# Performance work log

Hardware: AMD Instinct MI355X
Metric: run time of the kernel (lower is better)

The kernel has to match this reference:

```python
import jax, jax.numpy as jnp
import numpy as np
import math

B = 8; SEQ = 1000; C_IN = 32; D = 512; H = 8; DK = 64; DV = 64
DFF = 2048; NL = 4; ARY = 4; INNER = 5


def get_mask_np(seq_size, ary, inner):
    # full k-ary tree sizes (padded) and effective sizes per scale
    full = 1
    while full < seq_size:
        full *= ary
    all_size = [full]; effe = [seq_size]
    while all_size[-1] > 1:
        all_size.append(all_size[-1] // ary)
        effe.append(math.ceil(effe[-1] / ary))
    n = sum(all_size)
    allow = np.zeros((n, n), dtype=bool)
    w = inner // 2
    starts = np.concatenate([[0], np.cumsum(all_size)]).astype(int)
    # intra-scale local window
    for l, sz in enumerate(all_size):
        s = starts[l]
        for i in range(sz):
            lo = max(i - w, 0); hi = min(i + w + 1, sz)
            allow[s + i, s + lo:s + hi] = True
    # inter-scale parent<->children links
    for l in range(1, len(all_size)):
        s = starts[l]; ps = starts[l - 1]
        for i in range(all_size[l]):
            lo = ps + i * ary; hi = ps + (i + 1) * ary
            allow[s + i, lo:hi] = True
            allow[lo:hi, s + i] = True
    return allow, all_size, effe

ALLOW_NP, ALL_SIZE, EFFE_SIZE = get_mask_np(SEQ, ARY, INNER)
NTOT = sum(ALL_SIZE)   # 1365
DEPTH = len(ALL_SIZE)  # 6
OFFS = np.concatenate([[0], np.cumsum(ALL_SIZE)]).astype(int)


def sinusoid_pe(length, d):
    pos = np.arange(length)[:, None].astype(np.float64)
    i = np.arange(d)[None, :]
    ang = pos / np.power(10000.0, (2 * (i // 2)) / d)
    pe = np.zeros((length, d), np.float32)
    pe[:, 0::2] = np.sin(ang[:, 0::2]); pe[:, 1::2] = np.cos(ang[:, 1::2])
    return pe

PE_NP = sinusoid_pe(SEQ, D)


def layer_norm(x, s, b, eps=1e-5):
    m = x.mean(-1, keepdims=True)
    v = ((x - m) ** 2).mean(-1, keepdims=True)
    return (x - m) * jax.lax.rsqrt(v + eps) * s + b


def setup_inputs() -> dict:
    key = jax.random.key(0)
    ks = jax.random.split(key, 10)
    p = lambda k, shape, sc=0.02: jax.random.normal(k, shape, jnp.float32) * sc
    return {
        "x": jax.random.normal(ks[0], (B, SEQ, C_IN), jnp.float32),
        "conv_w": p(ks[1], (D, C_IN, 3), 0.05),
        "norm_s": jnp.ones((D,), jnp.float32), "norm_b": jnp.zeros((D,), jnp.float32),
        "wq": p(ks[2], (NL, D, H * DK)), "wk": p(ks[3], (NL, D, H * DK)),
        "wv": p(ks[4], (NL, D, H * DV)), "wo": p(ks[5], (NL, H * DV, D)),
        "ln1_s": jnp.ones((NL, D), jnp.float32), "ln1_b": jnp.zeros((NL, D), jnp.float32),
        "w1": p(ks[6], (NL, D, DFF)), "b1": jnp.zeros((NL, DFF), jnp.float32),
        "w2": p(ks[7], (NL, DFF, D)), "b2": jnp.zeros((NL, D), jnp.float32),
        "ln2_s": jnp.ones((NL, D), jnp.float32), "ln2_b": jnp.zeros((NL, D), jnp.float32),
    }


def reference(x, conv_w, norm_s, norm_b, wq, wk, wv, wo, ln1_s, ln1_b,
              w1, b1, w2, b2, ln2_s, ln2_b):
    allow = jnp.asarray(ALLOW_NP)        # [N,N] True = attend
    pe = jnp.asarray(PE_NP)              # [S,D]
    # --- DataEmbedding: conv1d(k=3, circular pad, no bias) + sinusoid PE ---
    xt = jnp.concatenate([x[:, -1:], x, x[:, :1]], axis=1)       # (B,S+2,C)
    emb = jax.lax.conv_general_dilated(
        xt, conv_w, (1,), 'VALID', dimension_numbers=('NWC', 'OIW', 'NWC'))
    emb = emb + pe[None]                                          # (B,S,D)
    # pad sequence to full-tree leaf count
    emb = jnp.pad(emb, ((0, 0), (0, ALL_SIZE[0] - SEQ), (0, 0)))  # (B,L0,D)
    # --- MaxPooling_Construct: pool by ary per level, concat, LayerNorm ---
    parts = [emb]
    cur = emb
    for lvl in range(DEPTH - 1):
        L = cur.shape[1]
        cur = cur.reshape(B, L // ARY, ARY, D).max(axis=2)
        parts.append(cur)
    seq = jnp.concatenate(parts, axis=1)                          # (B,N,D)
    seq = layer_norm(seq, norm_s, norm_b)
    # --- masked MHA encoder layers (post-norm) ---
    scale = 1.0 / math.sqrt(DK)
    neg = jnp.float32(-1e9)
    for l in range(NL):
        q = (seq @ wq[l]).reshape(B, NTOT, H, DK)
        k = (seq @ wk[l]).reshape(B, NTOT, H, DK)
        v = (seq @ wv[l]).reshape(B, NTOT, H, DV)
        scores = jnp.einsum('bnhd,bmhd->bhnm', q, k) * scale
        scores = jnp.where(allow[None, None], scores, neg)
        attn = jax.nn.softmax(scores, axis=-1)
        ctx = jnp.einsum('bhnm,bmhd->bnhd', attn, v).reshape(B, NTOT, H * DV)
        seq = layer_norm(seq + ctx @ wo[l], ln1_s[l], ln1_b[l])
        ff = jax.nn.gelu(seq @ w1[l] + b1[l], approximate=False) @ w2[l] + b2[l]
        seq = layer_norm(seq + ff, ln2_s[l], ln2_b[l])
    # --- keep only the effective (unpadded) prefix of each scale ---
    out = jnp.concatenate(
        [seq[:, OFFS[i]:OFFS[i] + EFFE_SIZE[i]] for i in range(DEPTH)], axis=1)
    return out  # (B, sum(effe)=1334, D)
```

## Files before the change

### kernel.cpp

```cpp
#include <hip/hip_runtime.h>
#include <cstdint>
#include <math.h>

#define DEV __device__ __forceinline__

static constexpr int BQ = 8, SEQN = 1000, CIN = 32, NH = 8;
static constexpr int NLAY = 4;
static constexpr int NTOT_C = 1365;
static constexpr int M_REAL = BQ * NTOT_C;
static constexpr int M_PAD  = 11008;

DEV float bf2f(unsigned short u){ return __uint_as_float(((unsigned)u) << 16); }
DEV unsigned short f2bf(float f){
  unsigned u = __float_as_uint(f);
  u += 0x7fffu + ((u >> 16) & 1u);
  return (unsigned short)(u >> 16);
}

typedef __bf16 bf16x8 __attribute__((ext_vector_type(8)));
typedef float  f32x4  __attribute__((ext_vector_type(4)));
typedef unsigned short u16x8 __attribute__((ext_vector_type(8)));

#define GLD_LDS16(gp, lp) __builtin_amdgcn_global_load_lds( \
    (const __attribute__((address_space(1))) void*)(gp), \
    (__attribute__((address_space(3))) void*)(lp), 16, 0, 0)

template<int N> DEV void waitcnt_vm(){
  asm volatile("s_waitcnt vmcnt(%0)" :: "i"(N) : "memory");
}
DEV void waitcnt_lgkm0(){ asm volatile("s_waitcnt lgkmcnt(0)" ::: "memory"); }
DEV void cfence(){ asm volatile("" ::: "memory"); }

DEV float gelu_f(float x){
  float z = 0.7978845608028654f * (x + 0.044715f * x * x * x);
  z = fminf(fmaxf(z, -10.f), 10.f);
  float e = __expf(2.f * z);
  float th = (e - 1.f) / (e + 1.f);
  return 0.5f * x * (1.f + th);
}

__global__ __launch_bounds__(256) void pe_kernel(float* __restrict__ pe)
{
  int idx = blockIdx.x * 256 + threadIdx.x;
  int d = idx & 511, s = idx >> 9;
  if (s >= SEQN) return;
  float e2 = (float)(d & ~1);
  float freq = exp2f(e2 * (-13.287712379549449f / 512.0f));
  float ang = (float)s * freq;
  pe[idx] = (d & 1) ? cosf(ang) : sinf(ang);
}

__global__ __launch_bounds__(256) void conv_kernel(const float* __restrict__ x,
    const float* __restrict__ w, const float* __restrict__ pe, float* __restrict__ seqf)
{
  __shared__ float ws_w[128 * 97];
  __shared__ __align__(16) float xs[66][32];
  int b = blockIdx.z, s0 = blockIdx.y * 64, d0 = blockIdx.x * 128;
  int tid = threadIdx.x;
  for (int i = tid; i < 128 * 96; i += 256){
    int r = i / 96, c = i - r * 96;
    ws_w[r * 97 + c] = w[(size_t)(d0 + r) * 96 + c];
  }
  for (int i = tid; i < 66 * 32; i += 256){
    int r = i >> 5, c = i & 31;
    int ss = s0 + r - 1;
    ss = (ss < 0) ? (ss + SEQN) : (ss >= SEQN ? ss - SEQN : ss);
    xs[r][c] = x[((size_t)b * SEQN + ss) * CIN + c];
  }
  __syncthreads();
  int dl = tid & 127, sh = tid >> 7;
  float wr[96];
  #pragma unroll
  for (int i = 0; i < 96; i++) wr[i] = ws_w[dl * 97 + i];
  int d = d0 + dl;
  for (int si = 0; si < 32; si++){
    int sl = sh * 32 + si;
    int s = s0 + sl;
    float acc = 0.f;
    #pragma unroll
    for (int kk = 0; kk < 3; kk++){
      const float* xr = xs[sl + kk];
      #pragma unroll
      for (int c = 0; c < 32; c++) acc += xr[c] * wr[c * 3 + kk];
    }
    float outv = (s < SEQN) ? acc + pe[(size_t)s * 512 + d] : 0.f;
    seqf[((size_t)b * NTOT_C + s) * 512 + d] = outv;
  }
}

__global__ __launch_bounds__(256) void pool_kernel(float* __restrict__ seqf,
    int inOff, int outOff, int outSz)
{
  int e = blockIdx.x * 256 + threadIdx.x;
  int d = e & 511;
  int r = e >> 9;
  int i = r % outSz;
  int b = r / outSz;
  const float* src = seqf + ((size_t)b * NTOT_C + inOff + 4 * i) * 512 + d;
  float m = fmaxf(fmaxf(src[0], src[512]), fmaxf(src[1024], src[1536]));
  seqf[((size_t)b * NTOT_C + outOff + i) * 512 + d] = m;
}

template<bool RES>
__global__ __launch_bounds__(256) void ln_kernel(const float* __restrict__ xin,
    const float* __restrict__ rin, float* __restrict__ outf, unsigned short* __restrict__ outb,
    const float* __restrict__ sg, const float* __restrict__ bg, int M)
{
  int row = blockIdx.x;
  int t = threadIdx.x;
  size_t base = (size_t)row * 512;
  if (row >= M){ outb[base + t] = 0; outb[base + t + 256] = 0; return; }
  float v0 = xin[base + t], v1 = xin[base + t + 256];
  if (RES){ v0 += rin[base + t]; v1 += rin[base + t + 256]; }
  __shared__ float red1[4], red2[4];
  int wv = t >> 6;
  float sall = v0 + v1;
  #pragma unroll
  for (int o = 32; o; o >>= 1) sall += __shfl_xor(sall, o, 64);
  if ((t & 63) == 0) red1[wv] = sall;
  __syncthreads();
  float mean = (red1[0] + red1[1] + red1[2] + red1[3]) * (1.f / 512.f);
  float d0 = v0 - mean, d1 = v1 - mean;
  float sq = d0 * d0 + d1 * d1;
  #pragma unroll
  for (int o = 32; o; o >>= 1) sq += __shfl_xor(sq, o, 64);
  if ((t & 63) == 0) red2[wv] = sq;
  __syncthreads();
  float var = (red2[0] + red2[1] + red2[2] + red2[3]) * (1.f / 512.f);
  float rstd = 1.f / sqrtf(var + 1e-5f);
  float y0 = d0 * rstd * sg[t] + bg[t];
  float y1 = d1 * rstd * sg[t + 256] + bg[t + 256];
  outf[base + t] = y0; outf[base + t + 256] = y1;
  outb[base + t] = f2bf(y0); outb[base + t + 256] = f2bf(y1);
}

__global__ __launch_bounds__(256) void wconv_kernel(const float* __restrict__ w,
    unsigned short* __restrict__ wt, int K, int N, size_t sStride, size_t dStride)
{
  __shared__ float tile[32][33];
  const float* wl = w + blockIdx.z * sStride;
  unsigned short* wtl = wt + blockIdx.z * dStride;
  int n0 = blockIdx.x * 32, k0 = blockIdx.y * 32;
  int c = threadIdx.x & 31, r8 = threadIdx.x >> 5;
  #pragma unroll
  for (int p = 0; p < 4; p++){ int r = r8 + p * 8; tile[r][c] = wl[(size_t)(k0 + r) * N + n0 + c]; }
  __syncthreads();
  #pragma unroll
  for (int p = 0; p < 4; p++){ int r = r8 + p * 8; wtl[(size_t)(n0 + r) * K + k0 + c] = f2bf(tile[c][r]); }
}

template<int EPI, int BM, int BN>
__global__ __launch_bounds__(256) void gemm2_kernel(
    const unsigned short* __restrict__ A, const unsigned short* __restrict__ Wt,
    float* __restrict__ Cf, unsigned short* __restrict__ Cb,
    const float* __restrict__ bias, const float* __restrict__ Rf, int N, int K)
{
  constexpr int MF = BM / 32, NF = BN / 32;
  constexpr int LA = BM / 32, LB = BN / 32;
  __shared__ __align__(16) unsigned short Abuf[2][BM * 64];
  __shared__ __align__(16) unsigned short Bbuf[2][BN * 64];
  const int tid = threadIdx.x;
  const int wid = tid >> 6, lane = tid & 63;
  const int wm2 = wid >> 1, wn2 = wid & 1;
  const int r16 = lane & 15, g = lane >> 4;
  const int m0 = blockIdx.x * BM, n0 = blockIdx.y * BN;

  const int row0 = tid >> 3;
  const int scol = ((tid & 7) ^ (row0 & 7)) * 8;
  const unsigned short* gAs = A  + (size_t)(m0 + row0) * K + scol;
  const unsigned short* gBs = Wt + (size_t)(n0 + row0) * K + scol;

  const int swz0 = ((0 + g) ^ (r16 & 7)) * 8;
  const int swz1 = ((4 + g) ^ (r16 & 7)) * 8;
  const int arow = (wm2 * (BM / 2) + r16) * 64;
  const int brow = (wn2 * (BN / 2) + r16) * 64;

  const int nt = K >> 6;
  f32x4 acc[MF][NF] = {};

  auto STAGE_A = [&](int buf, int kt){
    #pragma unroll
    for (int q = 0; q < LA; q++)
      GLD_LDS16(gAs + kt * 64 + (size_t)q * 32 * K, &Abuf[buf][q * 2048 + tid * 8]);
  };
  auto STAGE_B = [&](int buf, int kt){
    #pragma unroll
    for (int q = 0; q < LB; q++)
      GLD_LDS16(gBs + kt * 64 + (size_t)q * 32 * K, &Bbuf[buf][q * 2048 + tid * 8]);
  };

  cfence();
  STAGE_A(0, 0); STAGE_B(0, 0);
  if (nt > 1){ STAGE_A(1, 1); waitcnt_vm<LA>(); }
  else        { waitcnt_vm<0>(); }
  __builtin_amdgcn_s_barrier();
  cfence();

  for (int t = 0; t < nt; t++){
    const int d = t & 1;
    const unsigned short* Ab = Abuf[d];
    const unsigned short* Bb = Bbuf[d];

    bf16x8 a0[MF], b0[NF];
    #pragma unroll
    for (int m = 0; m < MF; m++) a0[m] = *reinterpret_cast<const bf16x8*>(&Ab[arow + m * 1024 + swz0]);
    #pragma unroll
    for (int n = 0; n < NF; n++) b0[n] = *reinterpret_cast<const bf16x8*>(&Bb[brow + n * 1024 + swz0]);
    if (t + 1 < nt){ cfence(); STAGE_B(d ^ 1, t + 1); cfence(); }
    __builtin_amdgcn_s_setprio(1);
    #pragma unroll
    for (int m = 0; m < MF; m++)
      #pragma unroll
      for (int n = 0; n < NF; n++)
        acc[m][n] = __builtin_amdgcn_mfma_f32_16x16x32_bf16(a0[m], b0[n], acc[m][n], 0, 0, 0);
    __builtin_amdgcn_s_setprio(0);

    bf16x8 a1[MF], b1v[NF];
    #pragma unroll
    for (int m = 0; m < MF; m++) a1[m] = *reinterpret_cast<const bf16x8*>(&Ab[arow + m * 1024 + swz1]);
    #pragma unroll
    for (int n = 0; n < NF; n++) b1v[n] = *reinterpret_cast<const bf16x8*>(&Bb[brow + n * 1024 + swz1]);
    waitcnt_lgkm0();
    __builtin_amdgcn_s_barrier();
    cfence();
    if (t + 2 < nt){ STAGE_A(d, t + 2); cfence(); }
    __builtin_amdgcn_s_setprio(1);
    #pragma unroll
    for (int m = 0; m < MF; m++)
      #pragma unroll
      for (int n = 0; n < NF; n++)
        acc[m][n] = __builtin_amdgcn_mfma_f32_16x16x32_bf16(a1[m], b1v[n], acc[m][n], 0, 0, 0);
    __builtin_amdgcn_s_setprio(0);

    if (t + 1 < nt){
      if (t + 2 < nt) waitcnt_vm<LA>();
      else            waitcnt_vm<0>();
      __builtin_amdgcn_s_barrier();
      cfence();
    }
  }

  const int colBase = n0 + wn2 * (BN / 2) + r16;
  #pragma unroll
  for (int m = 0; m < MF; m++){
    int row = m0 + wm2 * (BM / 2) + m * 16 + g * 4;
    #pragma unroll
    for (int n = 0; n < NF; n++){
      int col = colBase + n * 16;
      float bsv = (EPI >= 2) ? bias[col] : 0.f;
      #pragma unroll
      for (int j = 0; j < 4; j++){
        float v = acc[m][n][j];
        if (EPI >= 2) v += bsv;
        if (EPI == 2) v = gelu_f(v);
        size_t off = (size_t)(row + j) * N + col;
        if (EPI == 0 || EPI == 3) Cf[off] = v + Rf[off];
        else                      Cb[off] = f2bf(v);
      }
    }
  }
}

__global__ __launch_bounds__(256) void attn_kernel(
    const unsigned short* __restrict__ qkv, unsigned short* __restrict__ ctx)
{
  int wid = blockIdx.x * 4 + (threadIdx.x >> 6);
  int lane = threadIdx.x & 63;
  int n = wid % NTOT_C;
  int b = wid / NTOT_C;

  int i, sz, of, cb, par;
  if (n < 1024){ i = n;        sz = 1024; of = 0;    cb = -1;            par = 1024 + (i >> 2); }
  else if (n < 1280){ i = n - 1024; sz = 256; of = 1024; cb = 0    + 4 * i; par = 1280 + (i >> 2); }
  else if (n < 1344){ i = n - 1280; sz = 64;  of = 1280; cb = 1024 + 4 * i; par = 1344 + (i >> 2); }
  else if (n < 1360){ i = n - 1344; sz = 16;  of = 1344; cb = 1280 + 4 * i; par = 1360 + (i >> 2); }
  else if (n < 1364){ i = n - 1360; sz = 4;   of = 1360; cb = 1344 + 4 * i; par = 1364; }
  else { i = 0; sz = 1; of = 1364; cb = 1360; par = -1; }

  int nb[10];
  #pragma unroll
  for (int s5 = 0; s5 < 5; s5++){ int pos = i - 2 + s5; nb[s5] = (pos >= 0 && pos < sz) ? of + pos : -1; }
  #pragma unroll
  for (int r = 0; r < 4; r++) nb[5 + r] = (cb >= 0) ? cb + r : -1;
  nb[9] = par;

  const unsigned short* rows = qkv + ((size_t)b * NTOT_C) * 1536;

  u16x8 qv = *reinterpret_cast<const u16x8*>(rows + (size_t)n * 1536 + lane * 8);
  float qf[8];
  #pragma unroll
  for (int e = 0; e < 8; e++) qf[e] = bf2f(qv[e]);

  float sc[10];
  #pragma unroll
  for (int j = 0; j < 10; j++){
    int id = nb[j] >= 0 ? nb[j] : n;
    u16x8 kv = *reinterpret_cast<const u16x8*>(rows + (size_t)id * 1536 + 512 + lane * 8);
    float p = 0.f;
    #pragma unroll
    for (int e = 0; e < 8; e++) p += qf[e] * bf2f(kv[e]);
    p += __shfl_xor(p, 1, 64);
    p += __shfl_xor(p, 2, 64);
    p += __shfl_xor(p, 4, 64);
    sc[j] = (nb[j] >= 0) ? p * 0.125f : -1e30f;
  }
  float mx = sc[0];
  #pragma unroll
  for (int j = 1; j < 10; j++) mx = fmaxf(mx, sc[j]);
  float den = 0.f;
  float wj[10];
  #pragma unroll
  for (int j = 0; j < 10; j++){
    wj[j] = (nb[j] >= 0) ? expf(sc[j] - mx) : 0.f;
    den += wj[j];
  }
  float rden = 1.f / den;
  float accv[8] = {};
  #pragma unroll
  for (int j = 0; j < 10; j++){
    int id = nb[j] >= 0 ? nb[j] : n;
    u16x8 vv = *reinterpret_cast<const u16x8*>(rows + (size_t)id * 1536 + 1024 + lane * 8);
    float w = wj[j];
    #pragma unroll
    for (int e = 0; e < 8; e++) accv[e] += w * bf2f(vv[e]);
  }
  u16x8 ov;
  #pragma unroll
  for (int e = 0; e < 8; e++) ov[e] = f2bf(accv[e] * rden);
  *reinterpret_cast<u16x8*>(ctx + ((size_t)b * NTOT_C + n) * 512 + lane * 8) = ov;
}

__global__ __launch_bounds__(256) void gather_kernel(const float* __restrict__ seqf,
    float* __restrict__ out)
{
  int e = blockIdx.x * 256 + threadIdx.x;
  int d = e & 511;
  int r = e >> 9;
  int j = r % 1334;
  int b = r / 1334;
  int src;
  if      (j < 1000) src = j;
  else if (j < 1250) src = j + 24;
  else if (j < 1313) src = j + 30;
  else if (j < 1333) src = j + 31;
  else               src = 1364;
  out[e] = seqf[((size_t)b * NTOT_C + src) * 512 + d];
}

extern "C" void kernel_launch(void* const* d_in, const int* in_sizes, int n_in,
                              void* d_out, int out_size, void* d_ws, size_t ws_size,
                              hipStream_t stream)
{
  const float* x      = (const float*)d_in[0];
  const float* conv_w = (const float*)d_in[1];
  const float* norm_s = (const float*)d_in[2];
  const float* norm_b = (const float*)d_in[3];
  const float* wq     = (const float*)d_in[4];
  const float* wk     = (const float*)d_in[5];
  const float* wv     = (const float*)d_in[6];
  const float* wo     = (const float*)d_in[7];
  const float* ln1_s  = (const float*)d_in[8];
  const float* ln1_b  = (const float*)d_in[9];
  const float* w1     = (const float*)d_in[10];
  const float* b1     = (const float*)d_in[11];
  const float* w2     = (const float*)d_in[12];
  const float* b2     = (const float*)d_in[13];
  const float* ln2_s  = (const float*)d_in[14];
  const float* ln2_b  = (const float*)d_in[15];
  float* out = (float*)d_out;

  char* ws = (char*)d_ws;
  size_t off = 0;
  auto alloc = [&](size_t bytes) -> char* {
    char* p = ws + off; off += (bytes + 255) & ~(size_t)255; return p;
  };
  unsigned short* qkvT = (unsigned short*)alloc((size_t)NLAY * 1536 * 512 * 2);
  unsigned short* woT  = (unsigned short*)alloc((size_t)NLAY * 512 * 512 * 2);
  unsigned short* w1T  = (unsigned short*)alloc((size_t)NLAY * 2048 * 512 * 2);
  unsigned short* w2T  = (unsigned short*)alloc((size_t)NLAY * 512 * 2048 * 2);
  float*          seqf = (float*)alloc((size_t)M_PAD * 512 * 4);
  unsigned short* seqb = (unsigned short*)alloc((size_t)M_PAD * 512 * 2);
  float*          buff = (float*)alloc((size_t)M_PAD * 512 * 4);
  unsigned short* qkvb = (unsigned short*)alloc((size_t)M_PAD * 1536 * 2);
  unsigned short* ctxb = (unsigned short*)alloc((size_t)M_PAD * 512 * 2);
  unsigned short* ffn1 = qkvb;
  float*          pe   = buff;

  wconv_kernel<<<dim3(16,16,NLAY),256,0,stream>>>(wq, qkvT,              512,  512,  (size_t)512*512,  (size_t)1536*512);
  wconv_kernel<<<dim3(16,16,NLAY),256,0,stream>>>(wk, qkvT + 512*512,    512,  512,  (size_t)512*512,  (size_t)1536*512);
  wconv_kernel<<<dim3(16,16,NLAY),256,0,stream>>>(wv, qkvT + 1024*512,   512,  512,  (size_t)512*512,  (size_t)1536*512);
  wconv_kernel<<<dim3(16,16,NLAY),256,0,stream>>>(wo, woT,               512,  512,  (size_t)512*512,  (size_t)512*512);
  wconv_kernel<<<dim3(64,16,NLAY),256,0,stream>>>(w1, w1T,               512,  2048, (size_t)512*2048, (size_t)512*2048);
  wconv_kernel<<<dim3(16,64,NLAY),256,0,stream>>>(w2, w2T,               2048, 512,  (size_t)2048*512, (size_t)2048*512);

  pe_kernel<<<(SEQN * 512) / 256, 256, 0, stream>>>(pe);
  conv_kernel<<<dim3(4,16,BQ), 256, 0, stream>>>(x, conv_w, pe, seqf);
  const int psz[6]  = {1024, 256, 64, 16, 4, 1};
  const int poff[6] = {0, 1024, 1280, 1344, 1360, 1364};
  for (int l = 0; l < 5; l++)
    pool_kernel<<<(BQ * psz[l+1] * 512) / 256, 256, 0, stream>>>(seqf, poff[l], poff[l+1], psz[l+1]);
  ln_kernel<false><<<M_PAD, 256, 0, stream>>>(seqf, nullptr, seqf, seqb, norm_s, norm_b, M_REAL);

  for (int l = 0; l < NLAY; l++){
    gemm2_kernel<1,128,128><<<dim3(86,12),256,0,stream>>>(seqb, qkvT + (size_t)l*1536*512, nullptr, qkvb, nullptr, nullptr, 1536, 512);
    attn_kernel<<<(BQ * NTOT_C + 3) / 4, 256, 0, stream>>>(qkvb, ctxb);
    gemm2_kernel<0,64,128><<<dim3(172,4),256,0,stream>>>(ctxb, woT + (size_t)l*512*512, buff, nullptr, nullptr, seqf, 512, 512);
    ln_kernel<false><<<M_PAD,256,0,stream>>>(buff, nullptr, seqf, seqb, ln1_s + l*512, ln1_b + l*512, M_REAL);
    gemm2_kernel<2,128,128><<<dim3(86,16),256,0,stream>>>(seqb, w1T + (size_t)l*2048*512, nullptr, ffn1, b1 + l*2048, nullptr, 2048, 512);
    gemm2_kernel<3,64,128><<<dim3(172,4),256,0,stream>>>(ffn1, w2T + (size_t)l*512*2048, buff, nullptr, b2 + l*512, seqf, 512, 2048);
    ln_kernel<false><<<M_PAD,256,0,stream>>>(buff, nullptr, seqf, seqb, ln2_s + l*512, ln2_b + l*512, M_REAL);
  }

  gather_kernel<<<(BQ * 1334 * 512) / 256, 256, 0, stream>>>(seqf, out);
}
```

Before: 818.8 us.

## Fuse output-projection and FFN2 GEMMs with residual add and LayerNorm

Adds a gemmln kernel in which each block computes a full 64x512 output row tile, so the residual add, optional bias and LayerNorm can run in the GEMM epilogue and write seqf and seqb directly. This removes two separate LN kernel launches per layer and the fp32 intermediate buffer round trip. The trade-off is only 172 blocks with large accumulator tiles (32 accumulators per lane), a small K-tile of 32, and a large LDS B buffer, all of which may lower occupancy and GEMM efficiency. Padded rows in the initial LN now also zero the fp32 output so the fused residual reads stay clean.

```diff
diff --git a/kernel.cpp b/kernel.cpp
--- a/kernel.cpp
+++ b/kernel.cpp
@@ -109,7 +109,11 @@
   int row = blockIdx.x;
   int t = threadIdx.x;
   size_t base = (size_t)row * 512;
-  if (row >= M){ outb[base + t] = 0; outb[base + t + 256] = 0; return; }
+  if (row >= M){
+    outb[base + t] = 0; outb[base + t + 256] = 0;
+    outf[base + t] = 0.f; outf[base + t + 256] = 0.f;
+    return;
+  }
   float v0 = xin[base + t], v1 = xin[base + t + 256];
   if (RES){ v0 += rin[base + t]; v1 += rin[base + t + 256]; }
   __shared__ float red1[4], red2[4];
@@ -152,8 +156,7 @@
 template<int EPI, int BM, int BN>
 __global__ __launch_bounds__(256) void gemm2_kernel(
     const unsigned short* __restrict__ A, const unsigned short* __restrict__ Wt,
-    float* __restrict__ Cf, unsigned short* __restrict__ Cb,
-    const float* __restrict__ bias, const float* __restrict__ Rf, int N, int K)
+    unsigned short* __restrict__ Cb, const float* __restrict__ bias, int N, int K)
 {
   constexpr int MF = BM / 32, NF = BN / 32;
   constexpr int LA = BM / 32, LB = BN / 32;
@@ -247,15 +250,162 @@
     #pragma unroll
     for (int n = 0; n < NF; n++){
       int col = colBase + n * 16;
-      float bsv = (EPI >= 2) ? bias[col] : 0.f;
+      float bsv = (EPI == 2) ? bias[col] : 0.f;
       #pragma unroll
       for (int j = 0; j < 4; j++){
         float v = acc[m][n][j];
-        if (EPI >= 2) v += bsv;
-        if (EPI == 2) v = gelu_f(v);
-        size_t off = (size_t)(row + j) * N + col;
-        if (EPI == 0 || EPI == 3) Cf[off] = v + Rf[off];
-        else                      Cb[off] = f2bf(v);
+        if (EPI == 2) v = gelu_f(v + bsv);
+        Cb[(size_t)(row + j) * N + col] = f2bf(v);
+      }
+    }
+  }
+}
+
+template<bool HB>
+__global__ __launch_bounds__(256) void gemmln_kernel(
+    const unsigned short* __restrict__ A, const unsigned short* __restrict__ Wt,
+    float* __restrict__ seqf, unsigned short* __restrict__ seqb,
+    const float* __restrict__ bias, const float* __restrict__ sg,
+    const float* __restrict__ bg, int K)
+{
+  constexpr int LB = 8, L = 9;
+  __shared__ __align__(16) unsigned short Abuf[2][64 * 32];
+  __shared__ __align__(16) unsigned short Bbuf[2][512 * 32];
+  __shared__ float redS[64][2], redQ[64][2];
+  const int tid = threadIdx.x;
+  const int wid = tid >> 6, lane = tid & 63;
+  const int wm2 = wid >> 1, wn2 = wid & 1;
+  const int r16 = lane & 15, g = lane >> 4;
+  const int m0 = blockIdx.x * 64;
+
+  const int row0 = tid >> 2;
+  const int sc = ((tid & 3) ^ ((tid >> 3) & 3)) * 8;
+  const unsigned short* gAs = A  + (size_t)(m0 + row0) * K + sc;
+  const unsigned short* gBs = Wt + (size_t)row0 * K + sc;
+
+  const int nt = K >> 5;
+  f32x4 acc[2][16] = {};
+
+  auto STAGE = [&](int buf, int kt){
+    GLD_LDS16(gAs + kt * 32, &Abuf[buf][tid * 8]);
+    #pragma unroll
+    for (int q = 0; q < LB; q++)
+      GLD_LDS16(gBs + kt * 32 + (size_t)q * 64 * K, &Bbuf[buf][q * 2048 + tid * 8]);
+  };
+
+  cfence();
+  STAGE(0, 0);
+  const int swz = (g ^ ((r16 >> 1) & 3)) * 8;
+  const int aoff = (wm2 * 32 + r16) * 32 + swz;
+  const int boff = (wn2 * 256 + r16) * 32 + swz;
+
+  for (int t = 0; t < nt; t++){
+    const int d = t & 1;
+    if (t + 1 < nt){ STAGE(d ^ 1, t + 1); waitcnt_vm<L>(); }
+    else           { waitcnt_vm<0>(); }
+    __builtin_amdgcn_s_barrier();
+    cfence();
+    bf16x8 av[2], bv[16];
+    #pragma unroll
+    for (int m = 0; m < 2; m++)
+      av[m] = *reinterpret_cast<const bf16x8*>(&Abuf[d][aoff + m * 512]);
+    #pragma unroll
+    for (int n = 0; n < 16; n++)
+      bv[n] = *reinterpret_cast<const bf16x8*>(&Bbuf[d][boff + n * 512]);
+    __builtin_amdgcn_s_setprio(1);
+    #pragma unroll
+    for (int m = 0; m < 2; m++)
+      #pragma unroll
+      for (int n = 0; n < 16; n++)
+        acc[m][n] = __builtin_amdgcn_mfma_f32_16x16x32_bf16(av[m], bv[n], acc[m][n], 0, 0, 0);
+    __builtin_amdgcn_s_setprio(0);
+    waitcnt_lgkm0();
+    __builtin_amdgcn_s_barrier();
+    cfence();
+  }
+
+  const int colB = wn2 * 256 + r16;
+  #pragma unroll
+  for (int m = 0; m < 2; m++){
+    int row = m0 + wm2 * 32 + m * 16 + g * 4;
+    #pragma unroll
+    for (int n = 0; n < 16; n++){
+      int col = colB + n * 16;
+      float bsv = HB ? bias[col] : 0.f;
+      #pragma unroll
+      for (int j = 0; j < 4; j++)
+        acc[m][n][j] += bsv + seqf[(size_t)(row + j) * 512 + col];
+    }
+  }
+  float s[2][4];
+  #pragma unroll
+  for (int m = 0; m < 2; m++)
+    #pragma unroll
+    for (int j = 0; j < 4; j++){
+      float v = 0.f;
+      #pragma unroll
+      for (int n = 0; n < 16; n++) v += acc[m][n][j];
+      #pragma unroll
+      for (int o = 1; o < 16; o <<= 1) v += __shfl_xor(v, o, 64);
+      s[m][j] = v;
+    }
+  if (r16 == 0){
+    #pragma unroll
+    for (int m = 0; m < 2; m++)
+      #pragma unroll
+      for (int j = 0; j < 4; j++)
+        redS[wm2 * 32 + m * 16 + g * 4 + j][wn2] = s[m][j];
+  }
+  __syncthreads();
+  float meanv[2][4];
+  #pragma unroll
+  for (int m = 0; m < 2; m++)
+    #pragma unroll
+    for (int j = 0; j < 4; j++){
+      int rl = wm2 * 32 + m * 16 + g * 4 + j;
+      meanv[m][j] = (redS[rl][0] + redS[rl][1]) * (1.f / 512.f);
+    }
+  #pragma unroll
+  for (int m = 0; m < 2; m++)
+    #pragma unroll
+    for (int j = 0; j < 4; j++){
+      float v = 0.f;
+      #pragma unroll
+      for (int n = 0; n < 16; n++){ float dd = acc[m][n][j] - meanv[m][j]; v += dd * dd; }
+      #pragma unroll
+      for (int o = 1; o < 16; o <<= 1) v += __shfl_xor(v, o, 64);
+      s[m][j] = v;
+    }
+  if (r16 == 0){
+    #pragma unroll
+    for (int m = 0; m < 2; m++)
+      #pragma unroll
+      for (int j = 0; j < 4; j++)
+        redQ[wm2 * 32 + m * 16 + g * 4 + j][wn2] = s[m][j];
+  }
+  __syncthreads();
+  float rstdv[2][4];
+  #pragma unroll
+  for (int m = 0; m < 2; m++)
+    #pragma unroll
+    for (int j = 0; j < 4; j++){
+      int rl = wm2 * 32 + m * 16 + g * 4 + j;
+      float var = (redQ[rl][0] + redQ[rl][1]) * (1.f / 512.f);
+      rstdv[m][j] = 1.f / sqrtf(var + 1e-5f);
+    }
+  #pragma unroll
+  for (int m = 0; m < 2; m++){
+    int row = m0 + wm2 * 32 + m * 16 + g * 4;
+    #pragma unroll
+    for (int n = 0; n < 16; n++){
+      int col = colB + n * 16;
+      float sgv = sg[col], bgv = bg[col];
+      #pragma unroll
+      for (int j = 0; j < 4; j++){
+        float y = (acc[m][n][j] - meanv[m][j]) * rstdv[m][j] * sgv + bgv;
+        size_t off = (size_t)(row + j) * 512 + col;
+        seqf[off] = y;
+        seqb[off] = f2bf(y);
       }
     }
   }
@@ -380,7 +530,7 @@
   unsigned short* w2T  = (unsigned short*)alloc((size_t)NLAY * 512 * 2048 * 2);
   float*          seqf = (float*)alloc((size_t)M_PAD * 512 * 4);
   unsigned short* seqb = (unsigned short*)alloc((size_t)M_PAD * 512 * 2);
-  float*          buff = (float*)alloc((size_t)M_PAD * 512 * 4);
+  float*          buff = (float*)alloc((size_t)SEQN * 512 * 4);
   unsigned short* qkvb = (unsigned short*)alloc((size_t)M_PAD * 1536 * 2);
   unsigned short* ctxb = (unsigned short*)alloc((size_t)M_PAD * 512 * 2);
   unsigned short* ffn1 = qkvb;
@@ -402,13 +552,11 @@
   ln_kernel<false><<<M_PAD, 256, 0, stream>>>(seqf, nullptr, seqf, seqb, norm_s, norm_b, M_REAL);
 
   for (int l = 0; l < NLAY; l++){
-    gemm2_kernel<1,128,128><<<dim3(86,12),256,0,stream>>>(seqb, qkvT + (size_t)l*1536*512, nullptr, qkvb, nullptr, nullptr, 1536, 512);
+    gemm2_kernel<1,128,128><<<dim3(86,12),256,0,stream>>>(seqb, qkvT + (size_t)l*1536*512, qkvb, nullptr, 1536, 512);
     attn_kernel<<<(BQ * NTOT_C + 3) / 4, 256, 0, stream>>>(qkvb, ctxb);
-    gemm2_kernel<0,64,128><<<dim3(172,4),256,0,stream>>>(ctxb, woT + (size_t)l*512*512, buff, nullptr, nullptr, seqf, 512, 512);
-    ln_kernel<false><<<M_PAD,256,0,stream>>>(buff, nullptr, seqf, seqb, ln1_s + l*512, ln1_b + l*512, M_REAL);
-    gemm2_kernel<2,128,128><<<dim3(86,16),256,0,stream>>>(seqb, w1T + (size_t)l*2048*512, nullptr, ffn1, b1 + l*2048, nullptr, 2048, 512);
-    gemm2_kernel<3,64,128><<<dim3(172,4),256,0,stream>>>(ffn1, w2T + (size_t)l*512*2048, buff, nullptr, b2 + l*512, seqf, 512, 2048);
-    ln_kernel<false><<<M_PAD,256,0,stream>>>(buff, nullptr, seqf, seqb, ln2_s + l*512, ln2_b + l*512, M_REAL);
+    gemmln_kernel<false><<<172,256,0,stream>>>(ctxb, woT + (size_t)l*512*512, seqf, seqb, nullptr, ln1_s + l*512, ln1_b + l*512, 512);
+    gemm2_kernel<2,128,128><<<dim3(86,16),256,0,stream>>>(seqb, w1T + (size_t)l*2048*512, ffn1, b1 + l*2048, 2048, 512);
+    gemmln_kernel<true><<<172,256,0,stream>>>(ffn1, w2T + (size_t)l*512*2048, seqf, seqb, b2 + l*512, ln2_s + l*512, ln2_b + l*512, 2048);
   }
 
   gather_kernel<<<(BQ * 1334 * 512) / 256, 256, 0, stream>>>(seqf, out);
```

New measurement: 962.6 us. 1.18x slower.
